# Performance work log

Hardware: AMD Instinct MI355X
Metric: run time of the kernel (lower is better)

Reference implementation:

```python
import jax, jax.numpy as jnp
import numpy as np

H = 100  # hidden_state

def _lstm(x, W_ih, W_hh, b_ih, b_hh):
    # x: [B, T, D]; PyTorch gate order: i, f, g, o
    B, T, D = x.shape
    xg = jnp.einsum('btd,gd->btg', x, W_ih) + b_ih + b_hh  # [B, T, 4H]
    xg = jnp.transpose(xg, (1, 0, 2))  # [T, B, 4H]

    def step(carry, xt):
        h, c = carry
        g = xt + h @ W_hh.T
        i = jax.nn.sigmoid(g[:, 0*H:1*H])
        f = jax.nn.sigmoid(g[:, 1*H:2*H])
        gg = jnp.tanh(g[:, 2*H:3*H])
        o = jax.nn.sigmoid(g[:, 3*H:4*H])
        c = f * c + i * gg
        h = o * jnp.tanh(c)
        return (h, c), h

    h0 = jnp.zeros((B, H), x.dtype)
    c0 = jnp.zeros((B, H), x.dtype)
    _, hs = jax.lax.scan(step, (h0, c0), xg)  # [T, B, H]
    return jnp.transpose(hs, (1, 0, 2))  # [B, T, H]

def setup_inputs() -> dict:
    key = jax.random.key(0)
    ks = jax.random.split(key, 12)
    B, T, D, F = 64, 2048, 128, 300
    s = 1.0 / np.sqrt(H)
    u = lambda k, shape, sc: jax.random.uniform(k, shape, jnp.float32, -sc, sc)
    return {
        'x': jax.random.normal(ks[0], (B, T, D), jnp.float32),
        'y': jax.random.normal(ks[1], (B, T, D), jnp.float32),
        'W_ih': u(ks[2], (4 * H, D), s),
        'W_hh': u(ks[3], (4 * H, H), s),
        'b_ih': u(ks[4], (4 * H,), s),
        'b_hh': u(ks[5], (4 * H,), s),
        'ff1_w': u(ks[6], (F, H), 1.0 / np.sqrt(H)),
        'ff1_b': u(ks[7], (F,), 1.0 / np.sqrt(H)),
        'ff2_w': u(ks[8], (D, F), 1.0 / np.sqrt(F)),
        'ff2_b': u(ks[9], (D,), 1.0 / np.sqrt(F)),
    }

def reference(x, y, W_ih, W_hh, b_ih, b_hh, ff1_w, ff1_b, ff2_w, ff2_b):
    out = _lstm(x, W_ih, W_hh, b_ih, b_hh)          # [B, T, H]
    out = jax.nn.relu(out)
    out = jax.nn.relu(out @ ff1_w.T + ff1_b)         # [B, T, F]
    out = out @ ff2_w.T + ff2_b                      # [B, T, D]
    # training-mode forward returns out (e only updates running sigma stats)
    return out
```

## Files before the change

### kernel.cpp

```cpp
#include <hip/hip_runtime.h>
#include <math.h>

constexpr int H_ = 100;
constexpr int D_ = 128;
constexpr int F_ = 300;
constexpr int T_ = 2048;
constexpr int B_ = 64;
constexpr int G_ = 4 * H_;

#define KEEP4(v) asm volatile("" : "+v"(v.x), "+v"(v.y), "+v"(v.z), "+v"(v.w))

#define WL25(X) X(0) X(1) X(2) X(3) X(4) X(5) X(6) X(7) X(8) X(9) \
                X(10) X(11) X(12) X(13) X(14) X(15) X(16) X(17) X(18) X(19) \
                X(20) X(21) X(22) X(23) X(24)
#define WL32(X) WL25(X) X(25) X(26) X(27) X(28) X(29) X(30) X(31)

#define DECLW(i) float4 w##i = wp[i]; KEEP4(w##i);

#define LDOT(i) { float4 hv = *(const float4*)(hrow + 4*(i));                \
    a0 = fmaf(w##i.x, hv.x, a0); a1 = fmaf(w##i.y, hv.y, a1);                \
    a2 = fmaf(w##i.z, hv.z, a2); a3 = fmaf(w##i.w, hv.w, a3); }

#define ADOT(i) { float4 v0 = r0[i], v1 = r1[i], v2 = r2[i], v3 = r3[i];     \
  a0=fmaf(w##i.x,v0.x,a0); a0=fmaf(w##i.y,v0.y,a0);                          \
  a0=fmaf(w##i.z,v0.z,a0); a0=fmaf(w##i.w,v0.w,a0);                          \
  a1=fmaf(w##i.x,v1.x,a1); a1=fmaf(w##i.y,v1.y,a1);                          \
  a1=fmaf(w##i.z,v1.z,a1); a1=fmaf(w##i.w,v1.w,a1);                          \
  a2=fmaf(w##i.x,v2.x,a2); a2=fmaf(w##i.y,v2.y,a2);                          \
  a2=fmaf(w##i.z,v2.z,a2); a2=fmaf(w##i.w,v2.w,a2);                          \
  a3=fmaf(w##i.x,v3.x,a3); a3=fmaf(w##i.y,v3.y,a3);                          \
  a3=fmaf(w##i.z,v3.z,a3); a3=fmaf(w##i.w,v3.w,a3); }

static __device__ __forceinline__ float fast_rcp(float x) {
    return __builtin_amdgcn_rcpf(x);
}
static __device__ __forceinline__ float sigmoid_f(float u) {
    return fast_rcp(1.f + __expf(-u));
}
static __device__ __forceinline__ float tanh_safe(float c) {
    return fmaf(-2.f, fast_rcp(__expf(2.f * c) + 1.f), 1.f);
}

constexpr int AROWS = 32;

__global__ __launch_bounds__(512, 2) void xg_gemm(
    const float* __restrict__ x, const float* __restrict__ W_ih,
    const float* __restrict__ b_ih, const float* __restrict__ b_hh,
    float* __restrict__ xg)
{
    __shared__ float xs[AROWS * D_];
    const int tid = threadIdx.x;
    const long rowbase = (long)blockIdx.x * AROWS;

    {
        const float4* gx = (const float4*)(x + rowbase * D_);
        float4* sx = (float4*)xs;
        for (int i = tid; i < AROWS * D_ / 4; i += 512) sx[i] = gx[i];
    }
    __syncthreads();

    if (tid < G_) {
        const float4* wp = (const float4*)(W_ih + tid * D_);
        WL32(DECLW)
        const float bias = b_ih[tid] + b_hh[tid];

        #pragma unroll 1
        for (int g = 0; g < AROWS / 4; ++g) {
            float a0 = bias, a1 = bias, a2 = bias, a3 = bias;
            const float4* r0 = (const float4*)&xs[(4*g + 0) * D_];
            const float4* r1 = (const float4*)&xs[(4*g + 1) * D_];
            const float4* r2 = (const float4*)&xs[(4*g + 2) * D_];
            const float4* r3 = (const float4*)&xs[(4*g + 3) * D_];
            WL32(ADOT)
            float* orow = xg + (rowbase + 4*g) * G_ + tid;
            orow[0 * G_] = a0; orow[1 * G_] = a1;
            orow[2 * G_] = a2; orow[3 * G_] = a3;
        }
    }
}

__global__ __launch_bounds__(448, 1) void lstm_rec(
    const float* __restrict__ xg,
    const float* __restrict__ W_hh,
    float* __restrict__ hout)
{
    __shared__ float h_lds[2][128];
    const int tid  = threadIdx.x;
    const int lane = tid & 63;
    const int wv   = tid >> 6;
    const int g0   = lane >> 4;
    const int eo   = lane & 15;
    const int e    = wv * 16 + eo;
    const int ec   = (e < H_) ? e : (H_ - 1);
    const bool writer = (g0 == 0) && (e < H_);
    const int j    = g0 * H_ + ec;
    const float* xgb = xg + (long)blockIdx.x * T_ * G_ + j;
    float* hb = hout + (long)blockIdx.x * T_ * H_;

    const float4* wp = (const float4*)(W_hh + j * H_);
    WL25(DECLW)

    if (tid < H_) h_lds[0][tid] = 0.f;
    float c = 0.f;
    const bool isg = (g0 == 2);
    const bool sw0 = (g0 & 1) != 0;
    const bool sw1 = (g0 & 2) != 0;

    float p0 = xgb[0 * G_], p1 = xgb[1 * G_], p2 = xgb[2 * G_], p3 = xgb[3 * G_];
    __syncthreads();

#define STEP(PV, TIDX, RB, WB)                                               \
    {                                                                        \
        const float* hrow = &h_lds[RB][0];                                   \
        float a0 = (PV), a1 = 0.f, a2 = 0.f, a3 = 0.f;                       \
        WL25(LDOT)                                                           \
        float gv  = (a0 + a1) + (a2 + a3);                                   \
        float uu  = isg ? 2.f * gv : gv;                                     \
        float sg  = sigmoid_f(uu);                                           \
        float act = isg ? fmaf(2.f, sg, -1.f) : sg;     \
        float q1 = __shfl_xor(act, 16, 64);                                  \
        float q2 = __shfl_xor(act, 32, 64);                                  \
        float q3 = __shfl_xor(act, 48, 64);                                  \
        float t0 = sw0 ? q1 : act, t1 = sw0 ? act : q1;                      \
        float t2 = sw0 ? q3 : q2,  t3 = sw0 ? q2 : q3;                       \
        float gi = sw1 ? t2 : t0,  gf = sw1 ? t3 : t1;                       \
        float gG = sw1 ? t0 : t2,  go = sw1 ? t1 : t3;                       \
        c = fmaf(gf, c, gi * gG);                                            \
        float hv2 = go * tanh_safe(c);                                       \
        if (writer) {                                                        \
            h_lds[WB][e] = hv2;                                              \
            hb[(TIDX) * H_ + e] = hv2;                                       \
        }                                                                    \
        asm volatile("s_waitcnt lgkmcnt(0)" ::: "memory");                   \
        __builtin_amdgcn_s_barrier();                                        \
        asm volatile("" ::: "memory");                                       \
    }

    for (int t = 0; t < T_; t += 4) {
        float n0 = (t + 4 < T_) ? xgb[(t + 4) * G_] : 0.f;
        float n1 = (t + 5 < T_) ? xgb[(t + 5) * G_] : 0.f;
        float n2 = (t + 6 < T_) ? xgb[(t + 6) * G_] : 0.f;
        float n3 = (t + 7 < T_) ? xgb[(t + 7) * G_] : 0.f;
        STEP(p0, t + 0, 0, 1);
        STEP(p1, t + 1, 1, 0);
        STEP(p2, t + 2, 0, 1);
        STEP(p3, t + 3, 1, 0);
        p0 = n0; p1 = n1; p2 = n2; p3 = n3;
    }
#undef STEP
}

__global__ void prep_ff2(const float* __restrict__ ff2_w,
                         float* __restrict__ ff2_wP) {
    int i = blockIdx.x * 256 + threadIdx.x;
    if (i < D_ * F_) {
        int col = i / F_, k = i % F_;
        ff2_wP[((k >> 2) * D_ + col) * 4 + (k & 3)] = ff2_w[i];
    }
}

constexpr int CROWS = 32;

__global__ __launch_bounds__(512, 2) void ffn(
    const float* __restrict__ hin,
    const float* __restrict__ ff1_w, const float* __restrict__ ff1_b,
    const float* __restrict__ ff2_wP, const float* __restrict__ ff2_b,
    float* __restrict__ out)
{
    __shared__ float hs[CROWS * H_];
    __shared__ float fs[CROWS * F_];
    const int tid = threadIdx.x;
    const long rowbase = (long)blockIdx.x * CROWS;

    {
        const float4* gh = (const float4*)(hin + rowbase * H_);
        float4* sh = (float4*)hs;
        for (int i = tid; i < CROWS * H_ / 4; i += 512) {
            float4 v = gh[i];
            v.x = fmaxf(v.x, 0.f); v.y = fmaxf(v.y, 0.f);
            v.z = fmaxf(v.z, 0.f); v.w = fmaxf(v.w, 0.f);
            sh[i] = v;
        }
    }
    __syncthreads();

    if (tid < F_) {
        const float4* wp = (const float4*)(ff1_w + tid * H_);
        WL25(DECLW)
        const float bias = ff1_b[tid];
        #pragma unroll 1
        for (int g = 0; g < CROWS / 4; ++g) {
            float a0 = bias, a1 = bias, a2 = bias, a3 = bias;
            const float4* r0 = (const float4*)&hs[(4*g + 0) * H_];
            const float4* r1 = (const float4*)&hs[(4*g + 1) * H_];
            const float4* r2 = (const float4*)&hs[(4*g + 2) * H_];
            const float4* r3 = (const float4*)&hs[(4*g + 3) * H_];
            WL25(ADOT)
            fs[(4*g + 0) * F_ + tid] = fmaxf(a0, 0.f);
            fs[(4*g + 1) * F_ + tid] = fmaxf(a1, 0.f);
            fs[(4*g + 2) * F_ + tid] = fmaxf(a2, 0.f);
            fs[(4*g + 3) * F_ + tid] = fmaxf(a3, 0.f);
        }
    }
    __syncthreads();

    {
        const int col = tid & (D_ - 1);
        const int rg  = tid >> 7;
        const float4* wq = (const float4*)ff2_wP;
        const float bias = ff2_b[col];
        float acc[8];
        #pragma unroll
        for (int r = 0; r < 8; ++r) acc[r] = bias;

        #pragma unroll 5
        for (int k4 = 0; k4 < F_ / 4; ++k4) {
            float4 wv = wq[k4 * D_ + col];
            #pragma unroll
            for (int r = 0; r < 8; ++r) {
                const float4 v = *(const float4*)&fs[(rg * 8 + r) * F_ + 4 * k4];
                acc[r] = fmaf(wv.x, v.x, acc[r]);
                acc[r] = fmaf(wv.y, v.y, acc[r]);
                acc[r] = fmaf(wv.z, v.z, acc[r]);
                acc[r] = fmaf(wv.w, v.w, acc[r]);
            }
        }
        #pragma unroll
        for (int r = 0; r < 8; ++r)
            out[(rowbase + rg * 8 + r) * D_ + col] = acc[r];
    }
}

extern "C" void kernel_launch(void* const* d_in, const int* in_sizes, int n_in,
                              void* d_out, int out_size, void* d_ws, size_t ws_size,
                              hipStream_t stream) {
    const float* x     = (const float*)d_in[0];
    const float* W_ih  = (const float*)d_in[2];
    const float* W_hh  = (const float*)d_in[3];
    const float* b_ih  = (const float*)d_in[4];
    const float* b_hh  = (const float*)d_in[5];
    const float* ff1_w = (const float*)d_in[6];
    const float* ff1_b = (const float*)d_in[7];
    const float* ff2_w = (const float*)d_in[8];
    const float* ff2_b = (const float*)d_in[9];
    float* out = (float*)d_out;

    float* xg    = (float*)d_ws;
    float* hbuf  = xg + (long)B_ * T_ * G_;
    float* ff2wp = hbuf + (long)B_ * T_ * H_;

    prep_ff2<<<(D_ * F_ + 255) / 256, 256, 0, stream>>>(ff2_w, ff2wp);
    xg_gemm<<<(B_ * T_) / AROWS, 512, 0, stream>>>(x, W_ih, b_ih, b_hh, xg);
    lstm_rec<<<B_, 448, 0, stream>>>(xg, W_hh, hbuf);
    ffn<<<(B_ * T_) / CROWS, 512, 0, stream>>>(hbuf, ff1_w, ff1_b, ff2wp, ff2_b, out);
}
```

Measured before the change: 3.342 ms.

## Replace projection kernels with tiled GEMM and compute all four gates per thread in LSTM

The input projection and both feed-forward layers now use one templated 128x128 register-tiled GEMM staged through LDS, with fused bias and ReLU and zero-padded outputs. This replaces the weight-in-register row-dot kernels and the ff2 weight-repack kernel. The recurrence kernel now runs 128 threads per sequence, each holding all four gate rows of W_hh in registers. That removes the cross-lane shuffles and gate selection but gives each thread four times the serial FMA work per step and leaves fewer waves to spread across the SIMDs. The FFN intermediate reuses the xg workspace buffer.

```diff
diff --git a/kernel.cpp b/kernel.cpp
--- a/kernel.cpp
+++ b/kernel.cpp
@@ -7,29 +7,9 @@
 constexpr int T_ = 2048;
 constexpr int B_ = 64;
 constexpr int G_ = 4 * H_;
+constexpr long M_ = (long)B_ * T_;
 
 #define KEEP4(v) asm volatile("" : "+v"(v.x), "+v"(v.y), "+v"(v.z), "+v"(v.w))
-
-#define WL25(X) X(0) X(1) X(2) X(3) X(4) X(5) X(6) X(7) X(8) X(9) \
-                X(10) X(11) X(12) X(13) X(14) X(15) X(16) X(17) X(18) X(19) \
-                X(20) X(21) X(22) X(23) X(24)
-#define WL32(X) WL25(X) X(25) X(26) X(27) X(28) X(29) X(30) X(31)
-
-#define DECLW(i) float4 w##i = wp[i]; KEEP4(w##i);
-
-#define LDOT(i) { float4 hv = *(const float4*)(hrow + 4*(i));                \
-    a0 = fmaf(w##i.x, hv.x, a0); a1 = fmaf(w##i.y, hv.y, a1);                \
-    a2 = fmaf(w##i.z, hv.z, a2); a3 = fmaf(w##i.w, hv.w, a3); }
-
-#define ADOT(i) { float4 v0 = r0[i], v1 = r1[i], v2 = r2[i], v3 = r3[i];     \
-  a0=fmaf(w##i.x,v0.x,a0); a0=fmaf(w##i.y,v0.y,a0);                          \
-  a0=fmaf(w##i.z,v0.z,a0); a0=fmaf(w##i.w,v0.w,a0);                          \
-  a1=fmaf(w##i.x,v1.x,a1); a1=fmaf(w##i.y,v1.y,a1);                          \
-  a1=fmaf(w##i.z,v1.z,a1); a1=fmaf(w##i.w,v1.w,a1);                          \
-  a2=fmaf(w##i.x,v2.x,a2); a2=fmaf(w##i.y,v2.y,a2);                          \
-  a2=fmaf(w##i.z,v2.z,a2); a2=fmaf(w##i.w,v2.w,a2);                          \
-  a3=fmaf(w##i.x,v3.x,a3); a3=fmaf(w##i.y,v3.y,a3);                          \
-  a3=fmaf(w##i.z,v3.z,a3); a3=fmaf(w##i.w,v3.w,a3); }
 
 static __device__ __forceinline__ float fast_rcp(float x) {
     return __builtin_amdgcn_rcpf(x);
@@ -41,194 +21,173 @@
     return fmaf(-2.f, fast_rcp(__expf(2.f * c) + 1.f), 1.f);
 }
 
-constexpr int AROWS = 32;
-
-__global__ __launch_bounds__(512, 2) void xg_gemm(
-    const float* __restrict__ x, const float* __restrict__ W_ih,
-    const float* __restrict__ b_ih, const float* __restrict__ b_hh,
-    float* __restrict__ xg)
+template<int KTOT, int KB, int IN_LD, int W_LD, int OUT_LD, int N_REAL,
+         int WK_REAL, bool RELU_IN, bool RELU_OUT, bool SKIP_PAD_WRITE, bool BIAS2>
+__global__ __launch_bounds__(256, 2) void gemm128(
+    const float* __restrict__ Ain, const float* __restrict__ Wm,
+    const float* __restrict__ bias, const float* __restrict__ bias2,
+    float* __restrict__ Out)
 {
-    __shared__ float xs[AROWS * D_];
-    const int tid = threadIdx.x;
-    const long rowbase = (long)blockIdx.x * AROWS;
-
-    {
-        const float4* gx = (const float4*)(x + rowbase * D_);
-        float4* sx = (float4*)xs;
-        for (int i = tid; i < AROWS * D_ / 4; i += 512) sx[i] = gx[i];
+    __shared__ float as[KB][132];
+    __shared__ float bs[KB][132];
+    const int tid  = threadIdx.x;
+    const int lane = tid & 63;
+    const int wave = tid >> 6;
+    const int row0 = (wave >> 1) * 64 + (lane >> 3) * 8;
+    const int col0 = (wave & 1) * 64 + (lane & 7) * 8;
+    const long rb  = (long)blockIdx.x * 128;
+    const int  cb  = blockIdx.y * 128;
+    constexpr int K4 = KB / 4;
+
+    float acc[8][8];
+    #pragma unroll
+    for (int i = 0; i < 8; ++i)
+        #pragma unroll
+        for (int j = 0; j < 8; ++j) acc[i][j] = 0.f;
+
+    for (int kb = 0; kb < KTOT; kb += KB) {
+        for (int idx = tid; idx < 128 * K4; idx += 256) {
+            int row = idx / K4, k4 = idx % K4;
+            float4 v = *(const float4*)&Ain[(rb + row) * (long)IN_LD + kb + 4 * k4];
+            if constexpr (RELU_IN) {
+                v.x = fmaxf(v.x, 0.f); v.y = fmaxf(v.y, 0.f);
+                v.z = fmaxf(v.z, 0.f); v.w = fmaxf(v.w, 0.f);
+            }
+            as[4*k4+0][row] = v.x; as[4*k4+1][row] = v.y;
+            as[4*k4+2][row] = v.z; as[4*k4+3][row] = v.w;
+        }
+        for (int idx = tid; idx < 128 * K4; idx += 256) {
+            int col = idx / K4, k4 = idx % K4;
+            int gc = cb + col;
+            float4 v = make_float4(0.f, 0.f, 0.f, 0.f);
+            if (gc < N_REAL && (WK_REAL == KTOT || kb + 4 * k4 < WK_REAL))
+                v = *(const float4*)&Wm[(long)gc * W_LD + kb + 4 * k4];
+            bs[4*k4+0][col] = v.x; bs[4*k4+1][col] = v.y;
+            bs[4*k4+2][col] = v.z; bs[4*k4+3][col] = v.w;
+        }
+        __syncthreads();
+
+        #pragma unroll
+        for (int k = 0; k < KB; ++k) {
+            float4 a0 = *(const float4*)&as[k][row0];
+            float4 a1 = *(const float4*)&as[k][row0 + 4];
+            float4 b0 = *(const float4*)&bs[k][col0];
+            float4 b1 = *(const float4*)&bs[k][col0 + 4];
+            const float av[8] = {a0.x, a0.y, a0.z, a0.w, a1.x, a1.y, a1.z, a1.w};
+            const float bv[8] = {b0.x, b0.y, b0.z, b0.w, b1.x, b1.y, b1.z, b1.w};
+            #pragma unroll
+            for (int i = 0; i < 8; ++i)
+                #pragma unroll
+                for (int j = 0; j < 8; ++j)
+                    acc[i][j] = fmaf(av[i], bv[j], acc[i][j]);
+        }
+        __syncthreads();
     }
-    __syncthreads();
-
-    if (tid < G_) {
-        const float4* wp = (const float4*)(W_ih + tid * D_);
-        WL32(DECLW)
-        const float bias = b_ih[tid] + b_hh[tid];
-
-        #pragma unroll 1
-        for (int g = 0; g < AROWS / 4; ++g) {
-            float a0 = bias, a1 = bias, a2 = bias, a3 = bias;
-            const float4* r0 = (const float4*)&xs[(4*g + 0) * D_];
-            const float4* r1 = (const float4*)&xs[(4*g + 1) * D_];
-            const float4* r2 = (const float4*)&xs[(4*g + 2) * D_];
-            const float4* r3 = (const float4*)&xs[(4*g + 3) * D_];
-            WL32(ADOT)
-            float* orow = xg + (rowbase + 4*g) * G_ + tid;
-            orow[0 * G_] = a0; orow[1 * G_] = a1;
-            orow[2 * G_] = a2; orow[3 * G_] = a3;
+
+    #pragma unroll
+    for (int i = 0; i < 8; ++i) {
+        const long obase = (rb + row0 + i) * (long)OUT_LD + cb;
+        #pragma unroll
+        for (int j4 = 0; j4 < 2; ++j4) {
+            const int c0 = col0 + 4 * j4;
+            if (SKIP_PAD_WRITE && (cb + c0) >= N_REAL) continue;
+            float4 o;
+            float* oc = (float*)&o;
+            #pragma unroll
+            for (int j = 0; j < 4; ++j) {
+                const int cc = cb + c0 + j;
+                float v = acc[i][4 * j4 + j];
+                if (cc < N_REAL) {
+                    v += bias[cc];
+                    if constexpr (BIAS2) v += bias2[cc];
+                    if constexpr (RELU_OUT) v = fmaxf(v, 0.f);
+                } else {
+                    v = 0.f;
+                }
+                oc[j] = v;
+            }
+            *(float4*)&Out[obase + c0] = o;
         }
     }
 }
 
-__global__ __launch_bounds__(448, 1) void lstm_rec(
+#define FOR25(M) M(0) M(1) M(2) M(3) M(4) M(5) M(6) M(7) M(8) M(9) M(10) M(11) \
+                 M(12) M(13) M(14) M(15) M(16) M(17) M(18) M(19) M(20) M(21) M(22) M(23) M(24)
+
+__global__ __launch_bounds__(128, 1) void lstm_rec(
     const float* __restrict__ xg,
     const float* __restrict__ W_hh,
     float* __restrict__ hout)
 {
-    __shared__ float h_lds[2][128];
-    const int tid  = threadIdx.x;
-    const int lane = tid & 63;
-    const int wv   = tid >> 6;
-    const int g0   = lane >> 4;
-    const int eo   = lane & 15;
-    const int e    = wv * 16 + eo;
-    const int ec   = (e < H_) ? e : (H_ - 1);
-    const bool writer = (g0 == 0) && (e < H_);
-    const int j    = g0 * H_ + ec;
-    const float* xgb = xg + (long)blockIdx.x * T_ * G_ + j;
+    __shared__ float h_lds[2][104];
+    const int e  = threadIdx.x;
+    const int ec = (e < H_) ? e : (H_ - 1);
+    const bool act_lane = (e < H_);
+    const float* xgb = xg + (long)blockIdx.x * T_ * G_ + ec;
     float* hb = hout + (long)blockIdx.x * T_ * H_;
 
-    const float4* wp = (const float4*)(W_hh + j * H_);
-    WL25(DECLW)
-
-    if (tid < H_) h_lds[0][tid] = 0.f;
+    const float4* wp0 = (const float4*)(W_hh + (0 * H_ + ec) * H_);
+    const float4* wp1 = (const float4*)(W_hh + (1 * H_ + ec) * H_);
+    const float4* wp2 = (const float4*)(W_hh + (2 * H_ + ec) * H_);
+    const float4* wp3 = (const float4*)(W_hh + (3 * H_ + ec) * H_);
+#define DECLW4(i) \
+    float4 w0_##i = wp0[i]; KEEP4(w0_##i); float4 w1_##i = wp1[i]; KEEP4(w1_##i); \
+    float4 w2_##i = wp2[i]; KEEP4(w2_##i); float4 w3_##i = wp3[i]; KEEP4(w3_##i);
+    FOR25(DECLW4)
+
+    if (act_lane) h_lds[0][e] = 0.f;
     float c = 0.f;
-    const bool isg = (g0 == 2);
-    const bool sw0 = (g0 & 1) != 0;
-    const bool sw1 = (g0 & 2) != 0;
-
-    float p0 = xgb[0 * G_], p1 = xgb[1 * G_], p2 = xgb[2 * G_], p3 = xgb[3 * G_];
+
+    float4 p, q;
+    p.x = xgb[0];            p.y = xgb[H_];            p.z = xgb[2*H_];            p.w = xgb[3*H_];
+    q.x = xgb[G_];           q.y = xgb[G_+H_];         q.z = xgb[G_+2*H_];         q.w = xgb[G_+3*H_];
     __syncthreads();
 
-#define STEP(PV, TIDX, RB, WB)                                               \
-    {                                                                        \
-        const float* hrow = &h_lds[RB][0];                                   \
-        float a0 = (PV), a1 = 0.f, a2 = 0.f, a3 = 0.f;                       \
-        WL25(LDOT)                                                           \
-        float gv  = (a0 + a1) + (a2 + a3);                                   \
-        float uu  = isg ? 2.f * gv : gv;                                     \
-        float sg  = sigmoid_f(uu);                                           \
-        float act = isg ? fmaf(2.f, sg, -1.f) : sg;     \
-        float q1 = __shfl_xor(act, 16, 64);                                  \
-        float q2 = __shfl_xor(act, 32, 64);                                  \
-        float q3 = __shfl_xor(act, 48, 64);                                  \
-        float t0 = sw0 ? q1 : act, t1 = sw0 ? act : q1;                      \
-        float t2 = sw0 ? q3 : q2,  t3 = sw0 ? q2 : q3;                       \
-        float gi = sw1 ? t2 : t0,  gf = sw1 ? t3 : t1;                       \
-        float gG = sw1 ? t0 : t2,  go = sw1 ? t1 : t3;                       \
-        c = fmaf(gf, c, gi * gG);                                            \
-        float hv2 = go * tanh_safe(c);                                       \
-        if (writer) {                                                        \
-            h_lds[WB][e] = hv2;                                              \
-            hb[(TIDX) * H_ + e] = hv2;                                       \
-        }                                                                    \
-        asm volatile("s_waitcnt lgkmcnt(0)" ::: "memory");                   \
-        __builtin_amdgcn_s_barrier();                                        \
-        asm volatile("" ::: "memory");                                       \
-    }
-
-    for (int t = 0; t < T_; t += 4) {
-        float n0 = (t + 4 < T_) ? xgb[(t + 4) * G_] : 0.f;
-        float n1 = (t + 5 < T_) ? xgb[(t + 5) * G_] : 0.f;
-        float n2 = (t + 6 < T_) ? xgb[(t + 6) * G_] : 0.f;
-        float n3 = (t + 7 < T_) ? xgb[(t + 7) * G_] : 0.f;
-        STEP(p0, t + 0, 0, 1);
-        STEP(p1, t + 1, 1, 0);
-        STEP(p2, t + 2, 0, 1);
-        STEP(p3, t + 3, 1, 0);
-        p0 = n0; p1 = n1; p2 = n2; p3 = n3;
+#define KSTEP(i) { float4 hv = *(const float4*)&hr[4*(i)]; \
+    ac0.x = fmaf(w0_##i.x, hv.x, ac0.x); ac0.y = fmaf(w0_##i.y, hv.y, ac0.y); \
+    ac0.z = fmaf(w0_##i.z, hv.z, ac0.z); ac0.w = fmaf(w0_##i.w, hv.w, ac0.w); \
+    ac1.x = fmaf(w1_##i.x, hv.x, ac1.x); ac1.y = fmaf(w1_##i.y, hv.y, ac1.y); \
+    ac1.z = fmaf(w1_##i.z, hv.z, ac1.z); ac1.w = fmaf(w1_##i.w, hv.w, ac1.w); \
+    ac2.x = fmaf(w2_##i.x, hv.x, ac2.x); ac2.y = fmaf(w2_##i.y, hv.y, ac2.y); \
+    ac2.z = fmaf(w2_##i.z, hv.z, ac2.z); ac2.w = fmaf(w2_##i.w, hv.w, ac2.w); \
+    ac3.x = fmaf(w3_##i.x, hv.x, ac3.x); ac3.y = fmaf(w3_##i.y, hv.y, ac3.y); \
+    ac3.z = fmaf(w3_##i.z, hv.z, ac3.z); ac3.w = fmaf(w3_##i.w, hv.w, ac3.w); }
+
+#define STEP(PV, TIDX, RB, WB) { \
+    const float* hr = &h_lds[RB][0]; \
+    float4 ac0 = {PV.x, 0.f, 0.f, 0.f}; float4 ac1 = {PV.y, 0.f, 0.f, 0.f}; \
+    float4 ac2 = {PV.z, 0.f, 0.f, 0.f}; float4 ac3 = {PV.w, 0.f, 0.f, 0.f}; \
+    FOR25(KSTEP) \
+    float g0 = (ac0.x + ac0.y) + (ac0.z + ac0.w); \
+    float g1 = (ac1.x + ac1.y) + (ac1.z + ac1.w); \
+    float g2 = (ac2.x + ac2.y) + (ac2.z + ac2.w); \
+    float g3 = (ac3.x + ac3.y) + (ac3.z + ac3.w); \
+    float gi = sigmoid_f(g0), gf = sigmoid_f(g1), go = sigmoid_f(g3); \
+    float gt = fmaf(2.f, sigmoid_f(2.f * g2), -1.f);    \
+    c = fmaf(gf, c, gi * gt); \
+    float hv2 = go * tanh_safe(c); \
+    if (act_lane) { h_lds[WB][e] = hv2; hb[(long)(TIDX) * H_ + e] = hv2; } \
+    asm volatile("s_waitcnt lgkmcnt(0)" ::: "memory"); \
+    __builtin_amdgcn_s_barrier(); \
+    asm volatile("" ::: "memory"); }
+
+    for (int t = 0; t < T_; t += 2) {
+        float4 r4 = make_float4(0.f, 0.f, 0.f, 0.f);
+        float4 s4 = make_float4(0.f, 0.f, 0.f, 0.f);
+        if (t + 2 < T_) {
+            const long o = (long)(t + 2) * G_;
+            r4.x = xgb[o]; r4.y = xgb[o + H_]; r4.z = xgb[o + 2*H_]; r4.w = xgb[o + 3*H_];
+        }
+        if (t + 3 < T_) {
+            const long o = (long)(t + 3) * G_;
+            s4.x = xgb[o]; s4.y = xgb[o + H_]; s4.z = xgb[o + 2*H_]; s4.w = xgb[o + 3*H_];
+        }
+        STEP(p, t,     0, 1)
+        STEP(q, t + 1, 1, 0)
+        p = r4; q = s4;
     }
 #undef STEP
-}
-
-__global__ void prep_ff2(const float* __restrict__ ff2_w,
-                         float* __restrict__ ff2_wP) {
-    int i = blockIdx.x * 256 + threadIdx.x;
-    if (i < D_ * F_) {
-        int col = i / F_, k = i % F_;
-        ff2_wP[((k >> 2) * D_ + col) * 4 + (k & 3)] = ff2_w[i];
-    }
-}
-
-constexpr int CROWS = 32;
-
-__global__ __launch_bounds__(512, 2) void ffn(
-    const float* __restrict__ hin,
-    const float* __restrict__ ff1_w, const float* __restrict__ ff1_b,
-    const float* __restrict__ ff2_wP, const float* __restrict__ ff2_b,
-    float* __restrict__ out)
-{
-    __shared__ float hs[CROWS * H_];
-    __shared__ float fs[CROWS * F_];
-    const int tid = threadIdx.x;
-    const long rowbase = (long)blockIdx.x * CROWS;
-
-    {
-        const float4* gh = (const float4*)(hin + rowbase * H_);
-        float4* sh = (float4*)hs;
-        for (int i = tid; i < CROWS * H_ / 4; i += 512) {
-            float4 v = gh[i];
-            v.x = fmaxf(v.x, 0.f); v.y = fmaxf(v.y, 0.f);
-            v.z = fmaxf(v.z, 0.f); v.w = fmaxf(v.w, 0.f);
-            sh[i] = v;
-        }
-    }
-    __syncthreads();
-
-    if (tid < F_) {
-        const float4* wp = (const float4*)(ff1_w + tid * H_);
-        WL25(DECLW)
-        const float bias = ff1_b[tid];
-        #pragma unroll 1
-        for (int g = 0; g < CROWS / 4; ++g) {
-            float a0 = bias, a1 = bias, a2 = bias, a3 = bias;
-            const float4* r0 = (const float4*)&hs[(4*g + 0) * H_];
-            const float4* r1 = (const float4*)&hs[(4*g + 1) * H_];
-            const float4* r2 = (const float4*)&hs[(4*g + 2) * H_];
-            const float4* r3 = (const float4*)&hs[(4*g + 3) * H_];
-            WL25(ADOT)
-            fs[(4*g + 0) * F_ + tid] = fmaxf(a0, 0.f);
-            fs[(4*g + 1) * F_ + tid] = fmaxf(a1, 0.f);
-            fs[(4*g + 2) * F_ + tid] = fmaxf(a2, 0.f);
-            fs[(4*g + 3) * F_ + tid] = fmaxf(a3, 0.f);
-        }
-    }
-    __syncthreads();
-
-    {
-        const int col = tid & (D_ - 1);
-        const int rg  = tid >> 7;
-        const float4* wq = (const float4*)ff2_wP;
-        const float bias = ff2_b[col];
-        float acc[8];
-        #pragma unroll
-        for (int r = 0; r < 8; ++r) acc[r] = bias;
-
-        #pragma unroll 5
-        for (int k4 = 0; k4 < F_ / 4; ++k4) {
-            float4 wv = wq[k4 * D_ + col];
-            #pragma unroll
-            for (int r = 0; r < 8; ++r) {
-                const float4 v = *(const float4*)&fs[(rg * 8 + r) * F_ + 4 * k4];
-                acc[r] = fmaf(wv.x, v.x, acc[r]);
-                acc[r] = fmaf(wv.y, v.y, acc[r]);
-                acc[r] = fmaf(wv.z, v.z, acc[r]);
-                acc[r] = fmaf(wv.w, v.w, acc[r]);
-            }
-        }
-        #pragma unroll
-        for (int r = 0; r < 8; ++r)
-            out[(rowbase + rg * 8 + r) * D_ + col] = acc[r];
-    }
+#undef KSTEP
 }
 
 extern "C" void kernel_launch(void* const* d_in, const int* in_sizes, int n_in,
@@ -246,11 +205,17 @@
     float* out = (float*)d_out;
 
     float* xg    = (float*)d_ws;
-    float* hbuf  = xg + (long)B_ * T_ * G_;
-    float* ff2wp = hbuf + (long)B_ * T_ * H_;
-
-    prep_ff2<<<(D_ * F_ + 255) / 256, 256, 0, stream>>>(ff2_w, ff2wp);
-    xg_gemm<<<(B_ * T_) / AROWS, 512, 0, stream>>>(x, W_ih, b_ih, b_hh, xg);
-    lstm_rec<<<B_, 448, 0, stream>>>(xg, W_hh, hbuf);
-    ffn<<<(B_ * T_) / CROWS, 512, 0, stream>>>(hbuf, ff1_w, ff1_b, ff2wp, ff2_b, out);
-}
+    float* hbuf  = xg + M_ * G_;
+    float* g_ffn = xg;
+
+    gemm128<128, 32, 128, 128, 400, 400, 128, false, false, true, true>
+        <<<dim3(1024, 4), 256, 0, stream>>>(x, W_ih, b_ih, b_hh, xg);
+
+    lstm_rec<<<B_, 128, 0, stream>>>(xg, W_hh, hbuf);
+
+    gemm128<100, 20, 100, 100, 384, 300, 100, true, true, false, false>
+        <<<dim3(1024, 3), 256, 0, stream>>>(hbuf, ff1_w, ff1_b, nullptr, g_ffn);
+
+    gemm128<320, 32, 384, 300, 128, 128, 300, false, false, false, false>
+        <<<dim3(1024, 1), 256, 0, stream>>>(g_ffn, ff2_w, ff2_b, nullptr, out);
+}
```

Result: slower. 5.685 ms (+70.1%).
